# Optimization experiments

Measured on AMD Instinct MI355X. Metric: run time of the kernel, lower is better.

## Reference

```python
import jax, jax.numpy as jnp
import numpy as np


def setup_inputs() -> dict:
    key = jax.random.key(0)
    k1, k2 = jax.random.split(key)
    sat = jax.random.normal(k1, (96, 4, 64, 16), dtype=jnp.float32)
    grd = jax.random.normal(k2, (96, 4, 64, 16), dtype=jnp.float32)
    return {"sat_features": sat, "grd_features": grd}


def _corr(sat, grd):
    # sat: [Bs, h, W, c], grd: [Bg, h, Gw, c]
    Bs, h, W, c = sat.shape
    Bg, _, Gw, _ = grd.shape
    # circular pad along the width axis (dim 2), as in the torch code
    sat_pad = jnp.concatenate([sat, sat[:, :, : Gw - 1, :]], axis=2)  # [Bs,h,W+Gw-1,c]
    # torch flips grd along dim 3 (the c axis) before conv2d (cross-correlation)
    kern = grd[:, :, :, ::-1]  # [Bg,h,Gw,c] -> OIHW with O=Bg, I=h, H=Gw, W=c
    out = jax.lax.conv_general_dilated(
        sat_pad, kern, window_strides=(1, 1), padding='VALID',
        dimension_numbers=('NCHW', 'OIHW', 'NCHW'))  # [Bs,Bg,W,1]
    corr = out[..., 0]  # [Bs,Bg,W]
    orien = jnp.argmax(corr, axis=2).astype(jnp.int32)  # [Bs,Bg]
    return corr, orien


def reference(sat_features, grd_features):
    sat, grd = sat_features, grd_features
    Bs, h, W, c = sat.shape
    Bg, _, Gw, _ = grd.shape
    corr, orien = _corr(sat, grd)
    # per-pair circular shift + crop along width
    idx = (jnp.arange(Gw)[None, None, :] + orien[:, :, None]) % W  # [Bs,Bg,Gw]
    i_idx = jnp.arange(Bs)[:, None, None]  # broadcasts with idx
    sat_crop = sat[i_idx, :, idx, :]                # [Bs,Bg,Gw,h,c]
    sat_crop = jnp.transpose(sat_crop, (0, 1, 3, 2, 4))  # [Bs,Bg,h,Gw,c]
    norm = jnp.sqrt(jnp.sum(sat_crop ** 2, axis=(2, 3, 4), keepdims=True) + 1e-8)
    sat_matrix = sat_crop / norm
    dot = jnp.sum(sat_matrix * grd[None], axis=(2, 3, 4))  # [Bs,Bg]
    distance = 2.0 - 2.0 * dot.T                            # [Bg,Bs]
    return (sat_features, grd_features, distance, orien)
```

## Files before the change

### kernel.cpp

```cpp
#include <hip/hip_runtime.h>
#include <math.h>
#include <stdint.h>


#define BS   96
#define H    4
#define W    64
#define C    16
#define BG   96
#define HWC  (H*W*C)

#define SAT_ELEMS (BS*H*W*C)
#define OUT_DIST  (2*SAT_ELEMS)
#define OUT_ORIEN (OUT_DIST + BS*BG)

#define WS_NEEDED ((size_t)2 * SAT_ELEMS * 2)

typedef __attribute__((ext_vector_type(4)))  short short4v;
typedef __attribute__((ext_vector_type(8)))  short short8v;
typedef __attribute__((ext_vector_type(4)))  float f32x4;

__device__ __forceinline__ void bsplit(float x, unsigned short& hi, unsigned short& lo) {
    unsigned int u = __float_as_uint(x);
    unsigned int r = (u + 0x7FFFu + ((u >> 16) & 1u)) >> 16;
    hi = (unsigned short)r;
    float hf = __uint_as_float(r << 16);
    float l = x - hf;
    unsigned int ul = __float_as_uint(l);
    unsigned int rl = (ul + 0x7FFFu + ((ul >> 16) & 1u)) >> 16;
    lo = (unsigned short)rl;
}

__global__ __launch_bounds__(512)
void pf_pack_b(const float* __restrict__ sat, const float* __restrict__ grd,
               unsigned short* __restrict__ Bpk, float* __restrict__ out)
{
    int t = blockIdx.x * 512 + threadIdx.x;
    int lane = t & 63;
    int f    = t >> 6;
    int nt6  = f % 6;
    int g    = f / 6;
    int kh   = g & 1;
    int j    = g >> 1;

    int col = nt6 * 16 + (lane & 15);
    int u   = lane >> 4;
    int h   = kh * 2 + (u >> 1);
    int k0  = (u & 1) * 8;

    const float* row = grd + ((size_t)(col * 4 + h) * 64 + j) * 16 + (8 - k0);
    float tmp[8];
    *(float4*)&tmp[0] = *(const float4*)(row);
    *(float4*)&tmp[4] = *(const float4*)(row + 4);

    short8v hv, lv;
    #pragma unroll
    for (int e = 0; e < 8; ++e) {
        unsigned short hi, lo;
        bsplit(tmp[7 - e], hi, lo);
        hv[e] = (short)hi; lv[e] = (short)lo;
    }
    size_t base = (size_t)f << 10;
    *(short8v*)&Bpk[base + lane * 8]       = hv;
    *(short8v*)&Bpk[base + 512 + lane * 8] = lv;

    const float4* s4 = (const float4*)sat;
    const float4* g4 = (const float4*)grd;
    float4* o4 = (float4*)out;
    #pragma unroll
    for (int idx = t; idx < 2 * SAT_ELEMS / 4; idx += 49152) {
        o4[idx] = (idx < SAT_ELEMS / 4) ? s4[idx] : g4[idx - SAT_ELEMS / 4];
    }
}

#define MFMA16(a, b, c) __builtin_amdgcn_mfma_f32_16x16x32_bf16((a), (b), (c), 0, 0, 0)

__global__ __launch_bounds__(512, 4)
void pf_fused(const float* __restrict__ sat, const float* __restrict__ grd,
              const unsigned short* __restrict__ Bpk, float* __restrict__ out)
{
    __shared__ unsigned short sHi[4096], sLo[4096];
    __shared__ float corrPart[8][64][17];
    __shared__ float redW[8];
    __shared__ int   orienL[16];

    const int bs  = blockIdx.y;
    const int nt6 = blockIdx.x;
    const int bg0 = nt6 * 16;
    const int tid = threadIdx.x;
    const int wv  = tid >> 6, lane = tid & 63;
    const int u   = lane >> 4;
    const int kq  = wv;

    {
        const float4* satB = (const float4*)(sat + (size_t)bs * HWC);
        float np = 0.f;
        #pragma unroll
        for (int t = tid; t < 1024; t += 512) {
            float4 v = satB[t];
            int e = 4 * t;
            int h = e >> 10, w = (e >> 4) & 63, k = e & 15;
            int cc = (h * 16 + k) >> 3;
            int dst = w * 64 + ((cc ^ (w & 7)) * 8) + (k & 7);
            short4v hvv, lvv;
            unsigned short hi, lo;
            bsplit(v.x, hi, lo); hvv[0] = hi; lvv[0] = lo;
            bsplit(v.y, hi, lo); hvv[1] = hi; lvv[1] = lo;
            bsplit(v.z, hi, lo); hvv[2] = hi; lvv[2] = lo;
            bsplit(v.w, hi, lo); hvv[3] = hi; lvv[3] = lo;
            *(short4v*)&sHi[dst] = hvv;
            *(short4v*)&sLo[dst] = lvv;
            np = fmaf(v.x, v.x, fmaf(v.y, v.y, fmaf(v.z, v.z, fmaf(v.w, v.w, np))));
        }
        #pragma unroll
        for (int off = 32; off; off >>= 1) np += __shfl_xor(np, off);
        if (lane == 0) redW[wv] = np;
    }
    __syncthreads();

    f32x4 acc0 = {0.f,0.f,0.f,0.f}, acc1 = {0.f,0.f,0.f,0.f};
    f32x4 acc2 = {0.f,0.f,0.f,0.f}, acc3 = {0.f,0.f,0.f,0.f};

    const int l15 = lane & 15;
    const unsigned short* __restrict__ bb =
        Bpk + (((size_t)(kq * 8 * 2) * 6 + nt6) << 10) + lane * 8;

    short8v bh0 = *(const short8v*)(bb);
    short8v bl0 = *(const short8v*)(bb + 512);
    short8v bh1 = *(const short8v*)(bb + (6 << 10));
    short8v bl1 = *(const short8v*)(bb + (6 << 10) + 512);

    #define MT_STEP(ACC, mnum, J, BH0, BL0, BH1, BL1) { \
        const int r_ = ((mnum) * 16 + l15 + (J)) & 63; \
        const int base_ = r_ << 6; \
        const int rs_ = r_ & 7; \
        { const int aoff_ = base_ + (((u) ^ rs_) << 3); \
          short8v ah_ = *(const short8v*)&sHi[aoff_]; \
          short8v al_ = *(const short8v*)&sLo[aoff_]; \
          ACC = MFMA16(ah_, BH0, ACC); ACC = MFMA16(ah_, BL0, ACC); \
          ACC = MFMA16(al_, BH0, ACC); ACC = MFMA16(al_, BL0, ACC); } \
        { const int aoff_ = base_ + ((((4 + u)) ^ rs_) << 3); \
          short8v ah_ = *(const short8v*)&sHi[aoff_]; \
          short8v al_ = *(const short8v*)&sLo[aoff_]; \
          ACC = MFMA16(ah_, BH1, ACC); ACC = MFMA16(ah_, BL1, ACC); \
          ACC = MFMA16(al_, BH1, ACC); ACC = MFMA16(al_, BL1, ACC); } }

    #pragma unroll
    for (int jj = 0; jj < 8; ++jj) {
        const int j = kq * 8 + jj;
        short8v nh0, nl0, nh1, nl1;
        if (jj < 7) {
            const unsigned short* nb = bb + (size_t)(jj + 1) * (12 << 10);
            nh0 = *(const short8v*)(nb);
            nl0 = *(const short8v*)(nb + 512);
            nh1 = *(const short8v*)(nb + (6 << 10));
            nl1 = *(const short8v*)(nb + (6 << 10) + 512);
        }
        MT_STEP(acc0, 0, j, bh0, bl0, bh1, bl1);
        MT_STEP(acc1, 1, j, bh0, bl0, bh1, bl1);
        MT_STEP(acc2, 2, j, bh0, bl0, bh1, bl1);
        MT_STEP(acc3, 3, j, bh0, bl0, bh1, bl1);
        if (jj < 7) { bh0 = nh0; bl0 = nl0; bh1 = nh1; bl1 = nl1; }
    }
    #undef MT_STEP

    {
        const int rr = u * 4;
        #pragma unroll
        for (int reg = 0; reg < 4; ++reg) {
            corrPart[kq][rr + reg][l15]      = acc0[reg];
            corrPart[kq][16 + rr + reg][l15] = acc1[reg];
            corrPart[kq][32 + rr + reg][l15] = acc2[reg];
            corrPart[kq][48 + rr + reg][l15] = acc3[reg];
        }
    }
    __syncthreads();

    #pragma unroll
    for (int t = 0; t < 2; ++t) {
        const int bgc = wv * 2 + t;
        float v = ((corrPart[0][lane][bgc] + corrPart[1][lane][bgc])
                +  (corrPart[2][lane][bgc] + corrPart[3][lane][bgc]))
                + ((corrPart[4][lane][bgc] + corrPart[5][lane][bgc])
                +  (corrPart[6][lane][bgc] + corrPart[7][lane][bgc]));
        int idx = lane;
        #pragma unroll
        for (int off = 32; off; off >>= 1) {
            float ov = __shfl_xor(v, off);
            int   oi = __shfl_xor(idx, off);
            if (ov > v || (ov == v && oi < idx)) { v = ov; idx = oi; }
        }
        if (lane == 0) {
            orienL[bgc] = idx;
            out[OUT_ORIEN + bs * BG + bg0 + bgc] = (float)idx;
        }
    }
    __syncthreads();

    const float nrm = sqrtf(((redW[0] + redW[1]) + (redW[2] + redW[3]))
                          + ((redW[4] + redW[5]) + (redW[6] + redW[7])) + 1e-8f);

    #pragma unroll
    for (int t = 0; t < 2; ++t) {
        const int bgc = wv * 2 + t;
        const int bg = bg0 + bgc;
        const int r = (lane + orienL[bgc]) & 63;
        float s = 0.f;
        #pragma unroll
        for (int h = 0; h < 4; ++h) {
            const float4* sp = (const float4*)&sat[(((size_t)bs * 4 + h) * 64 + r) * 16];
            const float4* gp = (const float4*)&grd[(((size_t)bg * 4 + h) * 64 + lane) * 16];
            #pragma unroll
            for (int c4 = 0; c4 < 4; ++c4) {
                float4 sv = sp[c4];
                float4 gv = gp[c4];
                s = fmaf(sv.x, gv.x, fmaf(sv.y, gv.y, fmaf(sv.z, gv.z, fmaf(sv.w, gv.w, s))));
            }
        }
        #pragma unroll
        for (int off = 32; off; off >>= 1) s += __shfl_xor(s, off);
        if (lane == 0)
            out[OUT_DIST + (size_t)bg * BS + bs] = 2.f - 2.f * (s / nrm);
    }
}

__device__ __forceinline__ int satIdxFB(int hw, int c4) {
    return hw * 16 + 4 * ((c4 + (hw >> 1)) & 3);
}
__device__ __forceinline__ float rot_add(int baddr, float p) {
    return __int_as_float(__builtin_amdgcn_ds_bpermute(baddr, __float_as_int(p)));
}
__device__ __forceinline__ float dot_rev(const float4 s0, const float4 s1,
                                         const float4 s2, const float4 s3,
                                         const float* __restrict__ g) {
    float p0 = fmaf(s0.x, g[15], fmaf(s0.y, g[14], fmaf(s0.z, g[13], s0.w * g[12])));
    float p1 = fmaf(s1.x, g[11], fmaf(s1.y, g[10], fmaf(s1.z, g[ 9], s1.w * g[ 8])));
    float p2 = fmaf(s2.x, g[ 7], fmaf(s2.y, g[ 6], fmaf(s2.z, g[ 5], s2.w * g[ 4])));
    float p3 = fmaf(s3.x, g[ 3], fmaf(s3.y, g[ 2], fmaf(s3.z, g[ 1], s3.w * g[ 0])));
    return (p0 + p1) + (p2 + p3);
}
#define NB 8
__global__ __launch_bounds__(256)
void pf_fused_fb(const float* __restrict__ sat, const float* __restrict__ grd,
                 float* __restrict__ out)
{
    __shared__ float satL[H * W * C];
    __shared__ float partL[NB * 4 * W];
    __shared__ float sumL[4];
    __shared__ float dotP[NB * 4];
    __shared__ int   orienL[NB];
    const int bs = blockIdx.y, bg0 = blockIdx.x * NB;
    const int tid = threadIdx.x, wv = tid >> 6, lane = tid & 63;
    const float4* sp = (const float4*)(sat + (((size_t)bs * H + wv) * W + lane) * C);
    const float4 s0 = sp[0], s1 = sp[1], s2 = sp[2], s3 = sp[3];
    { const int hw = wv * W + lane;
      *(float4*)&satL[satIdxFB(hw,0)] = s0; *(float4*)&satL[satIdxFB(hw,1)] = s1;
      *(float4*)&satL[satIdxFB(hw,2)] = s2; *(float4*)&satL[satIdxFB(hw,3)] = s3; }
    { float a = fmaf(s0.x,s0.x,fmaf(s0.y,s0.y,fmaf(s0.z,s0.z,s0.w*s0.w)));
      float b = fmaf(s1.x,s1.x,fmaf(s1.y,s1.y,fmaf(s1.z,s1.z,s1.w*s1.w)));
      float c = fmaf(s2.x,s2.x,fmaf(s2.y,s2.y,fmaf(s2.z,s2.z,s2.w*s2.w)));
      float d = fmaf(s3.x,s3.x,fmaf(s3.y,s3.y,fmaf(s3.z,s3.z,s3.w*s3.w)));
      float s = (a+b)+(c+d);
      #pragma unroll
      for (int off = 32; off; off >>= 1) s += __shfl_xor(s, off);
      if (lane == 0) sumL[wv] = s; }
    const float* gpB = grd + (size_t)(bg0 * H + wv) * W * C;
    #pragma unroll
    for (int bp = 0; bp < NB/2; ++bp) {
        const float* gA = gpB + (2*bp) * HWC;
        const float* gB2 = gpB + (2*bp+1) * HWC;
        float accA = 0.f, accB = 0.f;
        int baddr = lane << 2;
        #pragma unroll 2
        for (int j = 0; j < W; ++j) {
            float pA = dot_rev(s0,s1,s2,s3, gA + j*C);
            float pB = dot_rev(s0,s1,s2,s3, gB2 + j*C);
            accA += rot_add(baddr, pA); accB += rot_add(baddr, pB);
            baddr = (baddr + 4) & 255;
        }
        partL[((2*bp)*4 + wv)*W + lane] = accA;
        partL[((2*bp+1)*4 + wv)*W + lane] = accB;
    }
    __syncthreads();
    for (int b = wv; b < NB; b += 4) {
        float v = (partL[(b*4+0)*W+lane] + partL[(b*4+1)*W+lane])
                + (partL[(b*4+2)*W+lane] + partL[(b*4+3)*W+lane]);
        int idx = lane;
        #pragma unroll
        for (int off = 32; off; off >>= 1) {
            float ov = __shfl_xor(v, off); int oi = __shfl_xor(idx, off);
            if (ov > v || (ov == v && oi < idx)) { v = ov; idx = oi; }
        }
        if (lane == 0) { orienL[b] = idx; out[OUT_ORIEN + bs*BG + (bg0+b)] = (float)idx; }
    }
    __syncthreads();
    const float nrm = sqrtf(sumL[0]+sumL[1]+sumL[2]+sumL[3] + 1e-8f);
    { float dp[NB];
      #pragma unroll
      for (int b = 0; b < NB; ++b) {
          const int row = (lane + orienL[b]) & 63;
          const float* gRow = grd + (((size_t)(bg0+b)*H + wv)*W + lane)*C;
          float s = 0.f;
          #pragma unroll
          for (int c4 = 0; c4 < 4; ++c4) {
              float4 sv = *(const float4*)&satL[satIdxFB(wv*W+row, c4)];
              float4 gv = *(const float4*)(gRow + 4*c4);
              s = fmaf(sv.x,gv.x, fmaf(sv.y,gv.y, fmaf(sv.z,gv.z, fmaf(sv.w,gv.w, s))));
          }
          dp[b] = s;
      }
      #pragma unroll
      for (int b = 0; b < NB; ++b) {
          float s = dp[b];
          #pragma unroll
          for (int off = 32; off; off >>= 1) s += __shfl_xor(s, off);
          if (lane == 0) dotP[b*4 + wv] = s;
      } }
    __syncthreads();
    if (tid < NB) {
        float d = ((dotP[tid*4+0]+dotP[tid*4+1])+(dotP[tid*4+2]+dotP[tid*4+3])) / nrm;
        out[OUT_DIST + (size_t)(bg0+tid)*BS + bs] = 2.f - 2.f*d;
    }
}

extern "C" void kernel_launch(void* const* d_in, const int* in_sizes, int n_in,
                              void* d_out, int out_size, void* d_ws, size_t ws_size,
                              hipStream_t stream) {
    const float* sat = (const float*)d_in[0];
    const float* grd = (const float*)d_in[1];
    float* out = (float*)d_out;

    if (ws_size < WS_NEEDED) {
        hipMemcpyAsync(out,             sat, (size_t)SAT_ELEMS * sizeof(float),
                       hipMemcpyDeviceToDevice, stream);
        hipMemcpyAsync(out + SAT_ELEMS, grd, (size_t)SAT_ELEMS * sizeof(float),
                       hipMemcpyDeviceToDevice, stream);
        dim3 grid(BG / NB, BS);
        pf_fused_fb<<<grid, 256, 0, stream>>>(sat, grd, out);
        return;
    }

    unsigned short* Bpk = (unsigned short*)d_ws;
    pf_pack_b<<<96, 512, 0, stream>>>(sat, grd, Bpk, out);
    pf_fused<<<dim3(6, BS), 512, 0, stream>>>(sat, grd, Bpk, out);
}
```

Before: 48.99 us.

## Split fused correlation kernel into split-K corr kernel plus epilogue kernel

```diff
diff --git a/kernel.cpp b/kernel.cpp
--- a/kernel.cpp
+++ b/kernel.cpp
@@ -14,7 +14,8 @@
 #define OUT_DIST  (2*SAT_ELEMS)
 #define OUT_ORIEN (OUT_DIST + BS*BG)
 
-#define WS_NEEDED ((size_t)2 * SAT_ELEMS * 2)
+#define WS_PART_OFF ((size_t)2 * SAT_ELEMS * 2)
+#define WS_NEEDED   (WS_PART_OFF + (size_t)1152 * 1024 * 4)
 
 typedef __attribute__((ext_vector_type(4)))  short short4v;
 typedef __attribute__((ext_vector_type(8)))  short short8v;
@@ -75,28 +76,25 @@
 
 #define MFMA16(a, b, c) __builtin_amdgcn_mfma_f32_16x16x32_bf16((a), (b), (c), 0, 0, 0)
 
-__global__ __launch_bounds__(512, 4)
-void pf_fused(const float* __restrict__ sat, const float* __restrict__ grd,
-              const unsigned short* __restrict__ Bpk, float* __restrict__ out)
+__global__ __launch_bounds__(256, 4)
+void pf_corr(const float* __restrict__ sat, const unsigned short* __restrict__ Bpk,
+             float* __restrict__ part)
 {
     __shared__ unsigned short sHi[4096], sLo[4096];
-    __shared__ float corrPart[8][64][17];
-    __shared__ float redW[8];
-    __shared__ int   orienL[16];
+    __shared__ float corrPart[4][64][17];
 
     const int bs  = blockIdx.y;
     const int nt6 = blockIdx.x;
-    const int bg0 = nt6 * 16;
+    const int kz  = blockIdx.z;
     const int tid = threadIdx.x;
     const int wv  = tid >> 6, lane = tid & 63;
-    const int u   = lane >> 4;
-    const int kq  = wv;
+    const int u   = lane >> 4, l15 = lane & 15;
+    const int kq  = kz * 4 + wv;
 
     {
         const float4* satB = (const float4*)(sat + (size_t)bs * HWC);
-        float np = 0.f;
-        #pragma unroll
-        for (int t = tid; t < 1024; t += 512) {
+        #pragma unroll
+        for (int t = tid; t < 1024; t += 256) {
             float4 v = satB[t];
             int e = 4 * t;
             int h = e >> 10, w = (e >> 4) & 63, k = e & 15;
@@ -110,25 +108,15 @@
             bsplit(v.w, hi, lo); hvv[3] = hi; lvv[3] = lo;
             *(short4v*)&sHi[dst] = hvv;
             *(short4v*)&sLo[dst] = lvv;
-            np = fmaf(v.x, v.x, fmaf(v.y, v.y, fmaf(v.z, v.z, fmaf(v.w, v.w, np))));
-        }
-        #pragma unroll
-        for (int off = 32; off; off >>= 1) np += __shfl_xor(np, off);
-        if (lane == 0) redW[wv] = np;
+        }
     }
     __syncthreads();
 
     f32x4 acc0 = {0.f,0.f,0.f,0.f}, acc1 = {0.f,0.f,0.f,0.f};
     f32x4 acc2 = {0.f,0.f,0.f,0.f}, acc3 = {0.f,0.f,0.f,0.f};
 
-    const int l15 = lane & 15;
     const unsigned short* __restrict__ bb =
         Bpk + (((size_t)(kq * 8 * 2) * 6 + nt6) << 10) + lane * 8;
-
-    short8v bh0 = *(const short8v*)(bb);
-    short8v bl0 = *(const short8v*)(bb + 512);
-    short8v bh1 = *(const short8v*)(bb + (6 << 10));
-    short8v bl1 = *(const short8v*)(bb + (6 << 10) + 512);
 
     #define MT_STEP(ACC, mnum, J, BH0, BL0, BH1, BL1) { \
         const int r_ = ((mnum) * 16 + l15 + (J)) & 63; \
@@ -148,19 +136,15 @@
     #pragma unroll
     for (int jj = 0; jj < 8; ++jj) {
         const int j = kq * 8 + jj;
-        short8v nh0, nl0, nh1, nl1;
-        if (jj < 7) {
-            const unsigned short* nb = bb + (size_t)(jj + 1) * (12 << 10);
-            nh0 = *(const short8v*)(nb);
-            nl0 = *(const short8v*)(nb + 512);
-            nh1 = *(const short8v*)(nb + (6 << 10));
-            nl1 = *(const short8v*)(nb + (6 << 10) + 512);
-        }
+        const unsigned short* bj = bb + (size_t)jj * (12 << 10);
+        short8v bh0 = *(const short8v*)(bj);
+        short8v bl0 = *(const short8v*)(bj + 512);
+        short8v bh1 = *(const short8v*)(bj + (6 << 10));
+        short8v bl1 = *(const short8v*)(bj + (6 << 10) + 512);
         MT_STEP(acc0, 0, j, bh0, bl0, bh1, bl1);
         MT_STEP(acc1, 1, j, bh0, bl0, bh1, bl1);
         MT_STEP(acc2, 2, j, bh0, bl0, bh1, bl1);
         MT_STEP(acc3, 3, j, bh0, bl0, bh1, bl1);
-        if (jj < 7) { bh0 = nh0; bl0 = nl0; bh1 = nh1; bl1 = nl1; }
     }
     #undef MT_STEP
 
@@ -168,21 +152,63 @@
         const int rr = u * 4;
         #pragma unroll
         for (int reg = 0; reg < 4; ++reg) {
-            corrPart[kq][rr + reg][l15]      = acc0[reg];
-            corrPart[kq][16 + rr + reg][l15] = acc1[reg];
-            corrPart[kq][32 + rr + reg][l15] = acc2[reg];
-            corrPart[kq][48 + rr + reg][l15] = acc3[reg];
-        }
-    }
-    __syncthreads();
-
-    #pragma unroll
-    for (int t = 0; t < 2; ++t) {
-        const int bgc = wv * 2 + t;
-        float v = ((corrPart[0][lane][bgc] + corrPart[1][lane][bgc])
-                +  (corrPart[2][lane][bgc] + corrPart[3][lane][bgc]))
-                + ((corrPart[4][lane][bgc] + corrPart[5][lane][bgc])
-                +  (corrPart[6][lane][bgc] + corrPart[7][lane][bgc]));
+            corrPart[wv][rr + reg][l15]      = acc0[reg];
+            corrPart[wv][16 + rr + reg][l15] = acc1[reg];
+            corrPart[wv][32 + rr + reg][l15] = acc2[reg];
+            corrPart[wv][48 + rr + reg][l15] = acc3[reg];
+        }
+    }
+    __syncthreads();
+
+    float* dst = part + ((size_t)((bs * 6 + nt6) * 2 + kz) << 10);
+    #pragma unroll
+    for (int e = tid; e < 1024; e += 256) {
+        const int row = e >> 4, col = e & 15;
+        dst[e] = (corrPart[0][row][col] + corrPart[1][row][col])
+               + (corrPart[2][row][col] + corrPart[3][row][col]);
+    }
+}
+
+__global__ __launch_bounds__(256)
+void pf_epi(const float* __restrict__ sat, const float* __restrict__ grd,
+            const float* __restrict__ part, float* __restrict__ out)
+{
+    __shared__ float corrE[64][17];
+    __shared__ float redW[4];
+    __shared__ int   orienL[16];
+
+    const int bs  = blockIdx.y;
+    const int nt6 = blockIdx.x;
+    const int bg0 = nt6 * 16;
+    const int tid = threadIdx.x;
+    const int wv  = tid >> 6, lane = tid & 63;
+
+    const float* p0 = part + ((size_t)((bs * 6 + nt6) * 2) << 10);
+    const float* p1 = p0 + 1024;
+    #pragma unroll
+    for (int e = tid; e < 1024; e += 256)
+        corrE[e >> 4][e & 15] = p0[e] + p1[e];
+
+    {
+        float np = 0.f;
+        const float4* sb = (const float4*)(sat + (size_t)bs * HWC);
+        #pragma unroll
+        for (int t = tid; t < 1024; t += 256) {
+            float4 v = sb[t];
+            np = fmaf(v.x, v.x, fmaf(v.y, v.y, fmaf(v.z, v.z, fmaf(v.w, v.w, np))));
+        }
+        #pragma unroll
+        for (int off = 32; off; off >>= 1) np += __shfl_xor(np, off);
+        if (lane == 0) redW[wv] = np;
+    }
+    __syncthreads();
+
+    const float nrm = sqrtf((redW[0] + redW[1]) + (redW[2] + redW[3]) + 1e-8f);
+
+    #pragma unroll
+    for (int t = 0; t < 4; ++t) {
+        const int bgc = wv * 4 + t;
+        float v = corrE[lane][bgc];
         int idx = lane;
         #pragma unroll
         for (int off = 32; off; off >>= 1) {
@@ -197,12 +223,9 @@
     }
     __syncthreads();
 
-    const float nrm = sqrtf(((redW[0] + redW[1]) + (redW[2] + redW[3]))
-                          + ((redW[4] + redW[5]) + (redW[6] + redW[7])) + 1e-8f);
-
-    #pragma unroll
-    for (int t = 0; t < 2; ++t) {
-        const int bgc = wv * 2 + t;
+    #pragma unroll
+    for (int t = 0; t < 4; ++t) {
+        const int bgc = wv * 4 + t;
         const int bg = bg0 + bgc;
         const int r = (lane + orienL[bgc]) & 63;
         float s = 0.f;
@@ -341,6 +364,9 @@
     }
 
     unsigned short* Bpk = (unsigned short*)d_ws;
+    float* part = (float*)((char*)d_ws + WS_PART_OFF);
+
     pf_pack_b<<<96, 512, 0, stream>>>(sat, grd, Bpk, out);
-    pf_fused<<<dim3(6, BS), 512, 0, stream>>>(sat, grd, Bpk, out);
-}
+    pf_corr<<<dim3(6, BS, 2), 256, 0, stream>>>(sat, Bpk, part);
+    pf_epi<<<dim3(6, BS), 256, 0, stream>>>(sat, grd, part, out);
+}
```

After: 53.87 us. +10.0%, slower.
